# Kernel optimization log

Hardware: AMD Instinct MI355X
Metric: run time of the kernel (lower is better)

The kernel has to match this reference:

```python
import jax, jax.numpy as jnp
import numpy as np

B, N, D_IN, E, H = 4, 512, 256, 64, 4
NEG = 1.0e9


def setup_inputs() -> dict:
    key = jax.random.key(0)
    ks = jax.random.split(key, 7)
    s = 1.0 / np.sqrt(D_IN)  # dense-init scale
    return {
        "x": jax.random.normal(ks[0], (B, N, D_IN), jnp.float32),
        "Wq": jax.random.normal(ks[1], (H, D_IN, E), jnp.float32) * s,
        "bq": jnp.zeros((H, E), jnp.float32),
        "Wk": jax.random.normal(ks[2], (H, D_IN, E), jnp.float32) * s,
        "bk": jnp.zeros((H, E), jnp.float32),
        "Wv": jax.random.normal(ks[3], (H, D_IN, E), jnp.float32) * s,
        "bv": jnp.zeros((H, E), jnp.float32),
    }


def _sdp(q, k, v):
    logits = jnp.einsum('bne,bme->bnm', q, k) / jnp.sqrt(jnp.asarray(E, q.dtype))
    return jnp.einsum('bnm,bme->bne', jax.nn.softmax(logits, axis=-1), v)


def _cosine(q, k, v):
    qn = q / jnp.linalg.norm(q, axis=-1, keepdims=True)
    kn = k / jnp.linalg.norm(k, axis=-1, keepdims=True)
    logits = jnp.einsum('bne,bme->bnm', qn, kn)
    return jnp.einsum('bnm,bme->bne', jax.nn.softmax(logits, axis=-1), v)


def _l1(q, k, v):
    # [B,N,N] L1 distances via broadcasted [B,N,N,E] diff, as in the original
    d = jnp.sum(jnp.abs(q[:, :, None, :] - k[:, None, :, :]), axis=-1)
    return jnp.einsum('bnm,bme->bne', jax.nn.softmax(-d, axis=-1), v)


def _l2(q, k, v):
    d = jnp.sqrt(jnp.sum(jnp.square(q[:, :, None, :] - k[:, None, :, :]), axis=-1))
    return jnp.einsum('bnm,bme->bne', jax.nn.softmax(-d, axis=-1), v)


_HEAD_FNS = (_sdp, _cosine, _l1, _l2)  # attention_types per head


def reference(x, Wq, bq, Wk, bk, Wv, bv):
    # Per-head projections: [B,H,N,E]
    q = jnp.einsum('bnd,hde->bhne', x, Wq) + bq[None, :, None, :]
    k = jnp.einsum('bnd,hde->bhne', x, Wk) + bk[None, :, None, :]
    v = jnp.einsum('bnd,hde->bhne', x, Wv) + bv[None, :, None, :]
    outs = [fn(q[:, h], k[:, h], v[:, h]) for h, fn in enumerate(_HEAD_FNS)]
    return jnp.concatenate(outs, axis=-1)  # [B,N,H*E]
```

## Files before the change

kernel.cpp:

```cpp
#include <hip/hip_runtime.h>
#include <hip/hip_bf16.h>
#include <math.h>

#define B_   4
#define N_   512
#define DIN  256
#define E_   64
#define H_   4

typedef __attribute__((ext_vector_type(8))) short bf16x8;
typedef __attribute__((ext_vector_type(8))) unsigned short u16x8;
typedef __attribute__((ext_vector_type(4))) float f32x4;

__device__ __forceinline__ unsigned short f2bf(float f) {
    __hip_bfloat16 h = __float2bfloat16(f);
    return *reinterpret_cast<unsigned short*>(&h);
}

__global__ __launch_bounds__(256) void proj_kernel(
    const float* __restrict__ x,
    const float* __restrict__ Wq, const float* __restrict__ bq,
    const float* __restrict__ Wk, const float* __restrict__ bk,
    const float* __restrict__ Wv, const float* __restrict__ bv,
    float* __restrict__ Q, float* __restrict__ KT,
    float* __restrict__ qn2, float* __restrict__ kn2,
    unsigned short* __restrict__ QF, unsigned short* __restrict__ KF,
    unsigned short* __restrict__ VF)
{
    const int tid = threadIdx.x;
    int blk = blockIdx.x;
    const int tile = blk & 15;  blk >>= 4;
    const int p    = blk % 3;   blk /= 3;
    const int h    = blk & 3;
    const int b    = blk >> 2;

    const float* W;
    const float* bias;
    if (p == 0)      { W = Wq; bias = bq; }
    else if (p == 1) { W = Wk; bias = bk; }
    else             { W = Wv; bias = bv; }
    W    += (size_t)h * DIN * E_;
    bias += h * E_;

    const int rowbase = tile * 32;
    const float* xb = x + ((size_t)b * N_ + rowbase) * DIN;

    __shared__ float XsT[64][34];
    __shared__ float Ws[64][64];
    __shared__ float Ys[64][33];
    __shared__ unsigned short Vst[64][40];

    const int tr = tid >> 4;
    const int tc = tid & 15;

    float acc[2][4];
    #pragma unroll
    for (int i = 0; i < 2; ++i)
        #pragma unroll
        for (int j = 0; j < 4; ++j) acc[i][j] = 0.f;

    for (int dc = 0; dc < DIN; dc += 64) {
        for (int l = tid; l < 2048; l += 256) {
            int r = l >> 6, d = l & 63;
            XsT[d][r] = xb[r * DIN + dc + d];
        }
        {
            const float4* Wg4 = (const float4*)(W + (size_t)dc * E_);
            #pragma unroll
            for (int i = 0; i < 4; ++i) ((float4*)Ws)[tid + i * 256] = Wg4[tid + i * 256];
        }
        __syncthreads();

        #pragma unroll 8
        for (int d = 0; d < 64; ++d) {
            float2 xv = *(const float2*)&XsT[d][tr * 2];
            float4 wv = *(const float4*)&Ws[d][tc * 4];
            acc[0][0] = fmaf(xv.x, wv.x, acc[0][0]);
            acc[0][1] = fmaf(xv.x, wv.y, acc[0][1]);
            acc[0][2] = fmaf(xv.x, wv.z, acc[0][2]);
            acc[0][3] = fmaf(xv.x, wv.w, acc[0][3]);
            acc[1][0] = fmaf(xv.y, wv.x, acc[1][0]);
            acc[1][1] = fmaf(xv.y, wv.y, acc[1][1]);
            acc[1][2] = fmaf(xv.y, wv.z, acc[1][2]);
            acc[1][3] = fmaf(xv.y, wv.w, acc[1][3]);
        }
        __syncthreads();
    }

    const size_t bh = (size_t)b * H_ + h;
    float4 bias4 = *(const float4*)&bias[tc * 4];
    float v0[4], v1[4];
    v0[0] = acc[0][0] + bias4.x; v0[1] = acc[0][1] + bias4.y;
    v0[2] = acc[0][2] + bias4.z; v0[3] = acc[0][3] + bias4.w;
    v1[0] = acc[1][0] + bias4.x; v1[1] = acc[1][1] + bias4.y;
    v1[2] = acc[1][2] + bias4.z; v1[3] = acc[1][3] + bias4.w;

    const int r0 = rowbase + tr * 2;

    if (p < 2) {
        float s0 = 0.f, s1 = 0.f;
        #pragma unroll
        for (int j = 0; j < 4; ++j) {
            s0 = fmaf(v0[j], v0[j], s0);
            s1 = fmaf(v1[j], v1[j], s1);
        }
        #pragma unroll
        for (int off = 1; off < 16; off <<= 1) {
            s0 += __shfl_xor(s0, off, 64);
            s1 += __shfl_xor(s1, off, 64);
        }
        if (tc == 0) {
            float* nrm = (p == 0) ? qn2 : kn2;
            nrm[bh * N_ + r0]     = s0;
            nrm[bh * N_ + r0 + 1] = s1;
        }
        unsigned short* f = ((p == 0) ? QF : KF) + bh * (size_t)(N_ * E_);
        const int t_ = r0 >> 4, li = r0 & 15;
        const int gg = tc >> 1, j0 = (tc & 1) * 4;
        ushort4 u0, u1;
        u0.x = f2bf(v0[0]); u0.y = f2bf(v0[1]); u0.z = f2bf(v0[2]); u0.w = f2bf(v0[3]);
        u1.x = f2bf(v1[0]); u1.y = f2bf(v1[1]); u1.z = f2bf(v1[2]); u1.w = f2bf(v1[3]);
        *(ushort4*)&f[(size_t)((t_ * 8 + gg) * 16 + li) * 8 + j0]       = u0;
        *(ushort4*)&f[(size_t)((t_ * 8 + gg) * 16 + li + 1) * 8 + j0]   = u1;
    }

    if (p == 0) {
        float* o = Q + bh * (size_t)(N_ * E_);
        *(float4*)&o[(size_t)r0 * E_ + tc * 4]       = make_float4(v0[0], v0[1], v0[2], v0[3]);
        *(float4*)&o[(size_t)(r0 + 1) * E_ + tc * 4] = make_float4(v1[0], v1[1], v1[2], v1[3]);
    } else if (p == 1) {
        #pragma unroll
        for (int j = 0; j < 4; ++j) {
            Ys[tc * 4 + j][tr * 2]     = v0[j];
            Ys[tc * 4 + j][tr * 2 + 1] = v1[j];
        }
        __syncthreads();
        const int e  = tid >> 2;
        const int n0 = (tid & 3) * 8;
        float* o = KT + bh * (size_t)(E_ * N_) + (size_t)e * N_ + rowbase + n0;
        float4 a, c;
        a.x = Ys[e][n0 + 0]; a.y = Ys[e][n0 + 1];
        a.z = Ys[e][n0 + 2]; a.w = Ys[e][n0 + 3];
        c.x = Ys[e][n0 + 4]; c.y = Ys[e][n0 + 5];
        c.z = Ys[e][n0 + 6]; c.w = Ys[e][n0 + 7];
        *(float4*)&o[0] = a;
        *(float4*)&o[4] = c;
    } else {
        #pragma unroll
        for (int j = 0; j < 4; ++j) {
            Vst[tc * 4 + j][tr * 2]     = f2bf(v0[j]);
            Vst[tc * 4 + j][tr * 2 + 1] = f2bf(v1[j]);
        }
        __syncthreads();
        const int et = tid >> 6, rem = tid & 63;
        const int g = rem >> 4, li = rem & 15;
        const int e = et * 16 + li, kb = rowbase >> 5;
        u16x8 wv8;
        #pragma unroll
        for (int j = 0; j < 8; ++j) wv8[j] = Vst[e][g * 8 + j];
        *(u16x8*)&VF[bh * (size_t)(N_ * E_)
                     + (size_t)(((et * 16 + kb) * 4 + g) * 16 + li) * 8] = wv8;
    }
}

template <int HEAD>
__device__ __forceinline__ void mfma_logits(
    int w, int lane, size_t bh, int qt, int q0,
    const unsigned short* __restrict__ QF,
    const unsigned short* __restrict__ KF,
    const float* __restrict__ qn2, const float* __restrict__ kn2,
    char* Pw, float (*wmax)[16], float (*wsum)[16])
{
    const int g = lane >> 4, li = lane & 15;
    const int row0 = g * 4;
    const unsigned short* qfb = QF + bh * (N_ * E_) + (size_t)qt * 1024;
    const unsigned short* kfb = KF + bh * (N_ * E_);

    bf16x8 a0 = *(const bf16x8*)&qfb[(g * 16 + li) * 8];
    bf16x8 a1 = *(const bf16x8*)&qfb[((g + 4) * 16 + li) * 8];

    float qrow[4];
    if (HEAD == 1) {
        #pragma unroll
        for (int j = 0; j < 4; ++j) qrow[j] = rsqrtf(qn2[bh * N_ + q0 + row0 + j]);
    } else if (HEAD == 3) {
        #pragma unroll
        for (int j = 0; j < 4; ++j) qrow[j] = qn2[bh * N_ + q0 + row0 + j];
    }

    float lg[8][4];
    #pragma unroll
    for (int t = 0; t < 8; ++t) {
        const int kt = w * 8 + t;
        const int m0 = kt * 16;
        bf16x8 b0 = *(const bf16x8*)&kfb[(size_t)((kt * 8 + g) * 16 + li) * 8];
        bf16x8 b1 = *(const bf16x8*)&kfb[(size_t)((kt * 8 + g + 4) * 16 + li) * 8];
        f32x4 acc = {0.f, 0.f, 0.f, 0.f};
        acc = __builtin_amdgcn_mfma_f32_16x16x32_bf16(a0, b0, acc, 0, 0, 0);
        acc = __builtin_amdgcn_mfma_f32_16x16x32_bf16(a1, b1, acc, 0, 0, 0);
        float kcol = 0.f, rk = 0.f;
        if (HEAD == 1) { kcol = kn2[bh * N_ + m0 + li]; rk = rsqrtf(kcol); }
        if (HEAD == 3) { kcol = kn2[bh * N_ + m0 + li]; }
        #pragma unroll
        for (int j = 0; j < 4; ++j) {
            float d = acc[j];
            if (HEAD == 0)      lg[t][j] = d * 0.125f;
            else if (HEAD == 1) lg[t][j] = d * qrow[j] * rk;
            else                lg[t][j] = -sqrtf(fmaxf(qrow[j] + kcol - 2.f * d, 0.f));
        }
    }

    float mx[4], gm[4];
    #pragma unroll
    for (int j = 0; j < 4; ++j) {
        float m = lg[0][j];
        #pragma unroll
        for (int t = 1; t < 8; ++t) m = fmaxf(m, lg[t][j]);
        #pragma unroll
        for (int off = 1; off < 16; off <<= 1) m = fmaxf(m, __shfl_xor(m, off, 64));
        mx[j] = m;
    }
    if (li == 0) {
        #pragma unroll
        for (int j = 0; j < 4; ++j) wmax[w][row0 + j] = mx[j];
    }
    __syncthreads();
    #pragma unroll
    for (int j = 0; j < 4; ++j)
        gm[j] = fmaxf(fmaxf(wmax[0][row0 + j], wmax[1][row0 + j]),
                      fmaxf(wmax[2][row0 + j], wmax[3][row0 + j]));

    float sm[4] = {0.f, 0.f, 0.f, 0.f};
    #pragma unroll
    for (int t = 0; t < 8; ++t) {
        #pragma unroll
        for (int j = 0; j < 4; ++j) {
            const int row = row0 + j;
            float pv = __expf(lg[t][j] - gm[j]);
            sm[j] += pv;
            const int byte = (row * 256 + (t * 16 + li) * 2) ^ ((row & 7) << 4);
            *(unsigned short*)(Pw + byte) = f2bf(pv);
        }
    }
    #pragma unroll
    for (int j = 0; j < 4; ++j) {
        float s = sm[j];
        #pragma unroll
        for (int off = 1; off < 16; off <<= 1) s += __shfl_xor(s, off, 64);
        if (li == 0) wsum[w][row0 + j] = s;
    }
}

__global__ __launch_bounds__(256) void attn_kernel(
    const float* __restrict__ Qf, const float* __restrict__ KT,
    const unsigned short* __restrict__ QF, const unsigned short* __restrict__ KF,
    const unsigned short* __restrict__ VF,
    const float* __restrict__ qn2, const float* __restrict__ kn2,
    float* __restrict__ out)
{
    const int tid  = threadIdx.x;
    const int w    = tid >> 6;
    const int lane = tid & 63;
    int blk = blockIdx.x;
    const int qt = blk & 31;
    const int h  = (blk >> 5) & 3;
    const int b  = blk >> 7;
    const size_t bh = (size_t)b * H_ + h;
    const int q0 = qt * 16;

    __shared__ unsigned short Plds[4][2048];
    __shared__ float part[4][16][68];
    __shared__ float wmax[4][16];
    __shared__ float wsum[4][16];
    __shared__ float q_lds[16][72];

    const int g = lane >> 4, li = lane & 15;
    char* Pw = (char*)&Plds[w][0];

    if (h == 2) {
        {
            const int i4 = tid * 4;
            const int r = i4 >> 6, c = i4 & 63;
            *(float4*)&q_lds[r][c] =
                *(const float4*)&Qf[bh * (N_ * E_) + (size_t)(q0 + r) * E_ + c];
        }
        __syncthreads();

        float acc0[16], acc1[16];
        #pragma unroll
        for (int r = 0; r < 16; ++r) { acc0[r] = 0.f; acc1[r] = 0.f; }

        const float* kp = KT + bh * (E_ * N_) + w * 128 + 2 * lane;
        for (int c = 0; c < 4; ++c) {
            float2 kk[16];
            #pragma unroll
            for (int i = 0; i < 16; ++i) kk[i] = *(const float2*)&kp[(c * 16 + i) * N_];
            #pragma unroll
            for (int r = 0; r < 16; ++r) {
                const float* qr = &q_lds[r][c * 16];
                float4 qa = *(const float4*)&qr[0];
                float4 qb = *(const float4*)&qr[4];
                float4 qc = *(const float4*)&qr[8];
                float4 qd = *(const float4*)&qr[12];
                float qv[16] = {qa.x, qa.y, qa.z, qa.w, qb.x, qb.y, qb.z, qb.w,
                                qc.x, qc.y, qc.z, qc.w, qd.x, qd.y, qd.z, qd.w};
                #pragma unroll
                for (int i = 0; i < 16; ++i) {
                    acc0[r] += fabsf(kk[i].x - qv[i]);
                    acc1[r] += fabsf(kk[i].y - qv[i]);
                }
            }
        }

        #pragma unroll
        for (int r = 0; r < 16; ++r) {
            float mn = fminf(acc0[r], acc1[r]);
            #pragma unroll
            for (int off = 1; off < 64; off <<= 1) mn = fminf(mn, __shfl_xor(mn, off, 64));
            if (lane == 0) wmax[w][r] = mn;
        }
        __syncthreads();
        #pragma unroll
        for (int r = 0; r < 16; ++r) {
            float gmn = fminf(fminf(wmax[0][r], wmax[1][r]), fminf(wmax[2][r], wmax[3][r]));
            float p0 = __expf(gmn - acc0[r]);
            float p1 = __expf(gmn - acc1[r]);
            float s = p0 + p1;
            #pragma unroll
            for (int off = 1; off < 64; off <<= 1) s += __shfl_xor(s, off, 64);
            if (lane == 0) wsum[w][r] = s;
            unsigned int pk = (unsigned int)f2bf(p0) | ((unsigned int)f2bf(p1) << 16);
            const int byte = (r * 256 + lane * 4) ^ ((r & 7) << 4);
            *(unsigned int*)(Pw + byte) = pk;
        }
    } else if (h == 0) {
        mfma_logits<0>(w, lane, bh, qt, q0, QF, KF, qn2, kn2, Pw, wmax, wsum);
    } else if (h == 1) {
        mfma_logits<1>(w, lane, bh, qt, q0, QF, KF, qn2, kn2, Pw, wmax, wsum);
    } else {
        mfma_logits<3>(w, lane, bh, qt, q0, QF, KF, qn2, kn2, Pw, wmax, wsum);
    }

    {
        bf16x8 pa[4];
        #pragma unroll
        for (int s = 0; s < 4; ++s) {
            const int byte = (li * 256 + (s * 32 + g * 8) * 2) ^ ((li & 7) << 4);
            pa[s] = *(const bf16x8*)(Pw + byte);
        }
        const unsigned short* vfb = VF + bh * (N_ * E_);
        const int row0 = g * 4;
        #pragma unroll
        for (int et = 0; et < 4; ++et) {
            f32x4 acc = {0.f, 0.f, 0.f, 0.f};
            #pragma unroll
            for (int s = 0; s < 4; ++s) {
                bf16x8 vb = *(const bf16x8*)&vfb[
                    (size_t)(((et * 16 + w * 4 + s) * 4 + g) * 16 + li) * 8];
                acc = __builtin_amdgcn_mfma_f32_16x16x32_bf16(pa[s], vb, acc, 0, 0, 0);
            }
            #pragma unroll
            for (int j = 0; j < 4; ++j) part[w][row0 + j][et * 16 + li] = acc[j];
        }
    }
    __syncthreads();

    #pragma unroll
    for (int k = 0; k < 4; ++k) {
        const int idx = tid + k * 256;
        const int row = idx >> 6, e = idx & 63;
        float s = part[0][row][e] + part[1][row][e] + part[2][row][e] + part[3][row][e];
        float rs = wsum[0][row] + wsum[1][row] + wsum[2][row] + wsum[3][row];
        out[((size_t)b * N_ + q0 + row) * (H_ * E_) + h * E_ + e] = s / rs;
    }
}

extern "C" void kernel_launch(void* const* d_in, const int* in_sizes, int n_in,
                              void* d_out, int out_size, void* d_ws, size_t ws_size,
                              hipStream_t stream)
{
    const float* x  = (const float*)d_in[0];
    const float* Wq = (const float*)d_in[1];
    const float* bq = (const float*)d_in[2];
    const float* Wk = (const float*)d_in[3];
    const float* bk = (const float*)d_in[4];
    const float* Wv = (const float*)d_in[5];
    const float* bv = (const float*)d_in[6];
    float* out = (float*)d_out;

    const size_t qkv = (size_t)B_ * H_ * N_ * E_;
    float* Q   = (float*)d_ws;
    float* KT  = Q + qkv;
    float* qn2 = KT + qkv;
    float* kn2 = qn2 + (size_t)B_ * H_ * N_;
    unsigned short* QF = (unsigned short*)(kn2 + (size_t)B_ * H_ * N_);
    unsigned short* KF = QF + qkv;
    unsigned short* VF = KF + qkv;

    proj_kernel<<<B_ * H_ * 3 * (N_ / 32), 256, 0, stream>>>(
        x, Wq, bq, Wk, bk, Wv, bv, Q, KT, qn2, kn2, QF, KF, VF);
    attn_kernel<<<B_ * H_ * (N_ / 16), 256, 0, stream>>>(
        Q, KT, QF, KF, VF, qn2, kn2, out);
}
```

Before: 57.79 us.

## Split attention over key chunks with flash-decoding style partial softmax combine

```diff
diff --git a/kernel.cpp b/kernel.cpp
--- a/kernel.cpp
+++ b/kernel.cpp
@@ -48,7 +48,7 @@
     __shared__ float XsT[64][34];
     __shared__ float Ws[64][64];
     __shared__ float Ys[64][33];
-    __shared__ unsigned short Vst[64][40];
+    __shared__ unsigned short Vst[64][48];
 
     const int tr = tid >> 4;
     const int tc = tid & 15;
@@ -152,24 +152,20 @@
             Vst[tc * 4 + j][tr * 2 + 1] = f2bf(v1[j]);
         }
         __syncthreads();
-        const int et = tid >> 6, rem = tid & 63;
-        const int g = rem >> 4, li = rem & 15;
-        const int e = et * 16 + li, kb = rowbase >> 5;
-        u16x8 wv8;
-        #pragma unroll
-        for (int j = 0; j < 8; ++j) wv8[j] = Vst[e][g * 8 + j];
+        const int et = tid >> 6, g = (tid >> 4) & 3, li = tid & 15;
+        u16x8 wv8 = *(const u16x8*)&Vst[et * 16 + li][g * 8];
         *(u16x8*)&VF[bh * (size_t)(N_ * E_)
-                     + (size_t)(((et * 16 + kb) * 4 + g) * 16 + li) * 8] = wv8;
+                     + (size_t)((((tile * 4 + et) * 4 + g) * 16) + li) * 8] = wv8;
     }
 }
 
 template <int HEAD>
-__device__ __forceinline__ void mfma_logits(
-    int w, int lane, size_t bh, int qt, int q0,
+__device__ __forceinline__ void mfma_logits32(
+    int w, int kh, int lane, size_t bh, int qt, int q0, int pid,
     const unsigned short* __restrict__ QF,
     const unsigned short* __restrict__ KF,
     const float* __restrict__ qn2, const float* __restrict__ kn2,
-    char* Pw, float (*wmax)[16], float (*wsum)[16])
+    char* Pw, float* __restrict__ Mpart, float* __restrict__ Spart)
 {
     const int g = lane >> 4, li = lane & 15;
     const int row0 = g * 4;
@@ -188,10 +184,10 @@
         for (int j = 0; j < 4; ++j) qrow[j] = qn2[bh * N_ + q0 + row0 + j];
     }
 
-    float lg[8][4];
+    float lg[2][4];
     #pragma unroll
-    for (int t = 0; t < 8; ++t) {
-        const int kt = w * 8 + t;
+    for (int t = 0; t < 2; ++t) {
+        const int kt = (kh * 4 + w) * 2 + t;
         const int m0 = kt * 16;
         bf16x8 b0 = *(const bf16x8*)&kfb[(size_t)((kt * 8 + g) * 16 + li) * 8];
         bf16x8 b1 = *(const bf16x8*)&kfb[(size_t)((kt * 8 + g + 4) * 16 + li) * 8];
@@ -210,35 +206,24 @@
         }
     }
 
-    float mx[4], gm[4];
+    float mx[4];
     #pragma unroll
     for (int j = 0; j < 4; ++j) {
-        float m = lg[0][j];
-        #pragma unroll
-        for (int t = 1; t < 8; ++t) m = fmaxf(m, lg[t][j]);
+        float m = fmaxf(lg[0][j], lg[1][j]);
         #pragma unroll
         for (int off = 1; off < 16; off <<= 1) m = fmaxf(m, __shfl_xor(m, off, 64));
         mx[j] = m;
     }
-    if (li == 0) {
-        #pragma unroll
-        for (int j = 0; j < 4; ++j) wmax[w][row0 + j] = mx[j];
-    }
-    __syncthreads();
-    #pragma unroll
-    for (int j = 0; j < 4; ++j)
-        gm[j] = fmaxf(fmaxf(wmax[0][row0 + j], wmax[1][row0 + j]),
-                      fmaxf(wmax[2][row0 + j], wmax[3][row0 + j]));
 
     float sm[4] = {0.f, 0.f, 0.f, 0.f};
     #pragma unroll
-    for (int t = 0; t < 8; ++t) {
+    for (int t = 0; t < 2; ++t) {
         #pragma unroll
         for (int j = 0; j < 4; ++j) {
             const int row = row0 + j;
-            float pv = __expf(lg[t][j] - gm[j]);
+            float pv = __expf(lg[t][j] - mx[j]);
             sm[j] += pv;
-            const int byte = (row * 256 + (t * 16 + li) * 2) ^ ((row & 7) << 4);
+            const int byte = (row * 64 + (t * 16 + li) * 2) ^ ((row & 7) << 4);
             *(unsigned short*)(Pw + byte) = f2bf(pv);
         }
     }
@@ -247,131 +232,172 @@
         float s = sm[j];
         #pragma unroll
         for (int off = 1; off < 16; off <<= 1) s += __shfl_xor(s, off, 64);
-        if (li == 0) wsum[w][row0 + j] = s;
-    }
-}
-
-__global__ __launch_bounds__(256) void attn_kernel(
+        if (li == 0) {
+            Mpart[(size_t)pid * 16 + row0 + j] = mx[j];
+            Spart[(size_t)pid * 16 + row0 + j] = s;
+        }
+    }
+}
+
+__global__ __launch_bounds__(256) void attn_partial(
     const float* __restrict__ Qf, const float* __restrict__ KT,
     const unsigned short* __restrict__ QF, const unsigned short* __restrict__ KF,
     const unsigned short* __restrict__ VF,
     const float* __restrict__ qn2, const float* __restrict__ kn2,
-    float* __restrict__ out)
+    float* __restrict__ Opart, float* __restrict__ Mpart,
+    float* __restrict__ Spart)
 {
     const int tid  = threadIdx.x;
     const int w    = tid >> 6;
     const int lane = tid & 63;
-    int blk = blockIdx.x;
-    const int qt = blk & 31;
-    const int h  = (blk >> 5) & 3;
-    const int b  = blk >> 7;
-    const size_t bh = (size_t)b * H_ + h;
+    const int blk  = blockIdx.x;
+    const int kh = blk & 3;
+    const int qt = (blk >> 2) & 31;
+    const int bh = blk >> 7;
+    const size_t bhs = (size_t)bh;
     const int q0 = qt * 16;
-
-    __shared__ unsigned short Plds[4][2048];
-    __shared__ float part[4][16][68];
-    __shared__ float wmax[4][16];
-    __shared__ float wsum[4][16];
-    __shared__ float q_lds[16][72];
+    const int pid = blk * 4 + w;
+
+    __shared__ unsigned short Plds[4][512];
+    __shared__ float q_lds[16][68];
 
     const int g = lane >> 4, li = lane & 15;
     char* Pw = (char*)&Plds[w][0];
+    const int h = bh & 3;
 
     if (h == 2) {
         {
-            const int i4 = tid * 4;
-            const int r = i4 >> 6, c = i4 & 63;
-            *(float4*)&q_lds[r][c] =
-                *(const float4*)&Qf[bh * (N_ * E_) + (size_t)(q0 + r) * E_ + c];
+            const int r = tid >> 4, c0 = (tid & 15) * 4;
+            *(float4*)&q_lds[r][c0] =
+                *(const float4*)&Qf[bhs * (N_ * E_) + (size_t)(q0 + r) * E_ + c0];
         }
         __syncthreads();
 
-        float acc0[16], acc1[16];
-        #pragma unroll
-        for (int r = 0; r < 16; ++r) { acc0[r] = 0.f; acc1[r] = 0.f; }
-
-        const float* kp = KT + bh * (E_ * N_) + w * 128 + 2 * lane;
-        for (int c = 0; c < 4; ++c) {
-            float2 kk[16];
+        const int half = lane >> 5;
+        const int kloc = lane & 31;
+        const int key  = kh * 128 + w * 32 + kloc;
+        const float* kp = KT + bhs * (E_ * N_) + key;
+
+        float acc[8];
+        #pragma unroll
+        for (int i = 0; i < 8; ++i) acc[i] = 0.f;
+
+        #pragma unroll 4
+        for (int ec = 0; ec < 16; ++ec) {
+            float k0 = kp[(size_t)(ec * 4 + 0) * N_];
+            float k1 = kp[(size_t)(ec * 4 + 1) * N_];
+            float k2 = kp[(size_t)(ec * 4 + 2) * N_];
+            float k3 = kp[(size_t)(ec * 4 + 3) * N_];
             #pragma unroll
-            for (int i = 0; i < 16; ++i) kk[i] = *(const float2*)&kp[(c * 16 + i) * N_];
+            for (int i = 0; i < 8; ++i) {
+                float4 q4 = *(const float4*)&q_lds[half * 8 + i][ec * 4];
+                acc[i] += fabsf(k0 - q4.x) + fabsf(k1 - q4.y)
+                        + fabsf(k2 - q4.z) + fabsf(k3 - q4.w);
+            }
+        }
+
+        #pragma unroll
+        for (int i = 0; i < 8; ++i) {
+            const int row = half * 8 + i;
+            float mn = acc[i];
             #pragma unroll
-            for (int r = 0; r < 16; ++r) {
-                const float* qr = &q_lds[r][c * 16];
-                float4 qa = *(const float4*)&qr[0];
-                float4 qb = *(const float4*)&qr[4];
-                float4 qc = *(const float4*)&qr[8];
-                float4 qd = *(const float4*)&qr[12];
-                float qv[16] = {qa.x, qa.y, qa.z, qa.w, qb.x, qb.y, qb.z, qb.w,
-                                qc.x, qc.y, qc.z, qc.w, qd.x, qd.y, qd.z, qd.w};
-                #pragma unroll
-                for (int i = 0; i < 16; ++i) {
-                    acc0[r] += fabsf(kk[i].x - qv[i]);
-                    acc1[r] += fabsf(kk[i].y - qv[i]);
-                }
+            for (int off = 1; off < 32; off <<= 1) mn = fminf(mn, __shfl_xor(mn, off, 64));
+            float m = -mn;
+            float p = __expf(mn - acc[i]);
+            float s = p;
+            #pragma unroll
+            for (int off = 1; off < 32; off <<= 1) s += __shfl_xor(s, off, 64);
+            const int byte = (row * 64 + kloc * 2) ^ ((row & 7) << 4);
+            *(unsigned short*)(Pw + byte) = f2bf(p);
+            if (kloc == 0) {
+                Mpart[(size_t)pid * 16 + row] = m;
+                Spart[(size_t)pid * 16 + row] = s;
             }
         }
-
-        #pragma unroll
-        for (int r = 0; r < 16; ++r) {
-            float mn = fminf(acc0[r], acc1[r]);
-            #pragma unroll
-            for (int off = 1; off < 64; off <<= 1) mn = fminf(mn, __shfl_xor(mn, off, 64));
-            if (lane == 0) wmax[w][r] = mn;
-        }
-        __syncthreads();
-        #pragma unroll
-        for (int r = 0; r < 16; ++r) {
-            float gmn = fminf(fminf(wmax[0][r], wmax[1][r]), fminf(wmax[2][r], wmax[3][r]));
-            float p0 = __expf(gmn - acc0[r]);
-            float p1 = __expf(gmn - acc1[r]);
-            float s = p0 + p1;
-            #pragma unroll
-            for (int off = 1; off < 64; off <<= 1) s += __shfl_xor(s, off, 64);
-            if (lane == 0) wsum[w][r] = s;
-            unsigned int pk = (unsigned int)f2bf(p0) | ((unsigned int)f2bf(p1) << 16);
-            const int byte = (r * 256 + lane * 4) ^ ((r & 7) << 4);
-            *(unsigned int*)(Pw + byte) = pk;
-        }
     } else if (h == 0) {
-        mfma_logits<0>(w, lane, bh, qt, q0, QF, KF, qn2, kn2, Pw, wmax, wsum);
+        mfma_logits32<0>(w, kh, lane, bhs, qt, q0, pid, QF, KF, qn2, kn2, Pw, Mpart, Spart);
     } else if (h == 1) {
-        mfma_logits<1>(w, lane, bh, qt, q0, QF, KF, qn2, kn2, Pw, wmax, wsum);
+        mfma_logits32<1>(w, kh, lane, bhs, qt, q0, pid, QF, KF, qn2, kn2, Pw, Mpart, Spart);
     } else {
-        mfma_logits<3>(w, lane, bh, qt, q0, QF, KF, qn2, kn2, Pw, wmax, wsum);
-    }
+        mfma_logits32<3>(w, kh, lane, bhs, qt, q0, pid, QF, KF, qn2, kn2, Pw, Mpart, Spart);
+    }
+    __syncthreads();
 
     {
-        bf16x8 pa[4];
-        #pragma unroll
-        for (int s = 0; s < 4; ++s) {
-            const int byte = (li * 256 + (s * 32 + g * 8) * 2) ^ ((li & 7) << 4);
-            pa[s] = *(const bf16x8*)(Pw + byte);
-        }
-        const unsigned short* vfb = VF + bh * (N_ * E_);
-        const int row0 = g * 4;
+        const int byte = (li * 64 + g * 16) ^ ((li & 7) << 4);
+        bf16x8 pa = *(const bf16x8*)(Pw + byte);
+        const int kb = kh * 4 + w;
+        const unsigned short* vfb = VF + bhs * (N_ * E_);
         #pragma unroll
         for (int et = 0; et < 4; ++et) {
             f32x4 acc = {0.f, 0.f, 0.f, 0.f};
-            #pragma unroll
-            for (int s = 0; s < 4; ++s) {
-                bf16x8 vb = *(const bf16x8*)&vfb[
-                    (size_t)(((et * 16 + w * 4 + s) * 4 + g) * 16 + li) * 8];
-                acc = __builtin_amdgcn_mfma_f32_16x16x32_bf16(pa[s], vb, acc, 0, 0, 0);
-            }
-            #pragma unroll
-            for (int j = 0; j < 4; ++j) part[w][row0 + j][et * 16 + li] = acc[j];
-        }
+            bf16x8 vb = *(const bf16x8*)&vfb[
+                (size_t)((((kb * 4 + et) * 4 + g) * 16) + li) * 8];
+            acc = __builtin_amdgcn_mfma_f32_16x16x32_bf16(pa, vb, acc, 0, 0, 0);
+            *(f32x4*)&Opart[(size_t)pid * 1024 + ((et * 4 + g) * 16 + li) * 4] = acc;
+        }
+    }
+}
+
+__global__ __launch_bounds__(256) void combine_kernel(
+    const float* __restrict__ Opart, const float* __restrict__ Mpart,
+    const float* __restrict__ Spart, float* __restrict__ out)
+{
+    const int tid = threadIdx.x;
+    const int blk = blockIdx.x;
+    const int qt = blk & 31, bh = blk >> 5;
+    const int b = bh >> 2, h = bh & 3;
+    const int base = blk * 16;
+
+    __shared__ float ms[16][16], ss[16][16], wls[16][16];
+    __shared__ float sginv[16];
+    __shared__ float Ot[16][68];
+
+    {
+        const int p = tid >> 4, row = tid & 15;
+        ms[p][row] = Mpart[(size_t)(base + p) * 16 + row];
+        ss[p][row] = Spart[(size_t)(base + p) * 16 + row];
     }
     __syncthreads();
-
-    #pragma unroll
-    for (int k = 0; k < 4; ++k) {
-        const int idx = tid + k * 256;
-        const int row = idx >> 6, e = idx & 63;
-        float s = part[0][row][e] + part[1][row][e] + part[2][row][e] + part[3][row][e];
-        float rs = wsum[0][row] + wsum[1][row] + wsum[2][row] + wsum[3][row];
-        out[((size_t)b * N_ + q0 + row) * (H_ * E_) + h * E_ + e] = s / rs;
+    {
+        const int p = tid >> 4, row = tid & 15;
+        float mg = ms[0][row];
+        #pragma unroll
+        for (int q = 1; q < 16; ++q) mg = fmaxf(mg, ms[q][row]);
+        wls[p][row] = __expf(ms[p][row] - mg);
+    }
+    __syncthreads();
+    if (tid < 16) {
+        float s = 0.f;
+        #pragma unroll
+        for (int p = 0; p < 16; ++p) s += wls[p][tid] * ss[p][tid];
+        sginv[tid] = 1.f / s;
+    }
+    __syncthreads();
+
+    {
+        const int et = tid >> 6, g = (tid >> 4) & 3, li = tid & 15;
+        float o0 = 0.f, o1 = 0.f, o2 = 0.f, o3 = 0.f;
+        const float* op = Opart + (size_t)base * 1024 + ((et * 4 + g) * 16 + li) * 4;
+        #pragma unroll
+        for (int p = 0; p < 16; ++p) {
+            float4 v = *(const float4*)(op + (size_t)p * 1024);
+            o0 = fmaf(wls[p][g * 4 + 0], v.x, o0);
+            o1 = fmaf(wls[p][g * 4 + 1], v.y, o1);
+            o2 = fmaf(wls[p][g * 4 + 2], v.z, o2);
+            o3 = fmaf(wls[p][g * 4 + 3], v.w, o3);
+        }
+        Ot[g * 4 + 0][et * 16 + li] = o0 * sginv[g * 4 + 0];
+        Ot[g * 4 + 1][et * 16 + li] = o1 * sginv[g * 4 + 1];
+        Ot[g * 4 + 2][et * 16 + li] = o2 * sginv[g * 4 + 2];
+        Ot[g * 4 + 3][et * 16 + li] = o3 * sginv[g * 4 + 3];
+    }
+    __syncthreads();
+    {
+        const int row = tid >> 4, e0 = (tid & 15) * 4;
+        const int n = qt * 16 + row;
+        *(float4*)&out[((size_t)b * N_ + n) * (H_ * E_) + h * E_ + e0] =
+            *(const float4*)&Ot[row][e0];
     }
 }
 
@@ -389,16 +415,20 @@
     float* out = (float*)d_out;
 
     const size_t qkv = (size_t)B_ * H_ * N_ * E_;
-    float* Q   = (float*)d_ws;
-    float* KT  = Q + qkv;
-    float* qn2 = KT + qkv;
-    float* kn2 = qn2 + (size_t)B_ * H_ * N_;
-    unsigned short* QF = (unsigned short*)(kn2 + (size_t)B_ * H_ * N_);
+    float* Q     = (float*)d_ws;
+    float* KT    = Q + qkv;
+    float* qn2   = KT + qkv;
+    float* kn2   = qn2 + (size_t)B_ * H_ * N_;
+    float* Opart = kn2 + (size_t)B_ * H_ * N_;
+    float* Mpart = Opart + (size_t)8192 * 1024;
+    float* Spart = Mpart + (size_t)8192 * 16;
+    unsigned short* QF = (unsigned short*)(Spart + (size_t)8192 * 16);
     unsigned short* KF = QF + qkv;
     unsigned short* VF = KF + qkv;
 
     proj_kernel<<<B_ * H_ * 3 * (N_ / 32), 256, 0, stream>>>(
         x, Wq, bq, Wk, bk, Wv, bv, Q, KT, qn2, kn2, QF, KF, VF);
-    attn_kernel<<<B_ * H_ * (N_ / 16), 256, 0, stream>>>(
-        Q, KT, QF, KF, VF, qn2, kn2, out);
-}
+    attn_partial<<<B_ * H_ * 32 * 4, 256, 0, stream>>>(
+        Q, KT, QF, KF, VF, qn2, kn2, Opart, Mpart, Spart);
+    combine_kernel<<<B_ * H_ * 32, 256, 0, stream>>>(Opart, Mpart, Spart, out);
+}
```

Result: faster. 53.96 us (-6.6%).
